# Kernel tuning notes

Measured on AMD Instinct MI355X. Metric: run time of the kernel, lower is better.

Reference implementation:

```python
import jax, jax.numpy as jnp
import numpy as np

B, T, H, N = 4, 2048, 16, 64  # batch, seq, heads, head_size (RWKV standard N=64)


def setup_inputs() -> dict:
    key = jax.random.key(0)
    ks = jax.random.split(key, 5)
    r = jax.random.normal(ks[0], (B, T, H, N), jnp.float32)
    k = jax.random.normal(ks[1], (B, T, H, N), jnp.float32)
    v = jax.random.normal(ks[2], (B, T, H, N), jnp.float32)
    w = jax.random.normal(ks[3], (B, T, H, N), jnp.float32)  # raw decay logits
    u = jax.random.normal(ks[4], (H, N), jnp.float32)         # per-head bonus
    return {"r": r, "k": k, "v": v, "w": w, "u": u}


def _wkv_scan(r, k, v, w, u):
    # RWKV-6 fused recurrent WKV.
    # decay in (0,1): exp(-exp(w)) per RWKV-6 parameterization
    decay = jnp.exp(-jnp.exp(w))  # [B,T,H,N]
    # time-major for lax.scan: [T,B,H,N]
    rt = jnp.moveaxis(r, 1, 0)
    kt = jnp.moveaxis(k, 1, 0)
    vt = jnp.moveaxis(v, 1, 0)
    dt = jnp.moveaxis(decay, 1, 0)
    S0 = jnp.zeros((r.shape[0], r.shape[2], r.shape[3], r.shape[3]), r.dtype)  # [B,H,N,N]

    ub = u[None]  # [1,H,N] broadcast over batch; key index i gets bonus

    def step(S, x):
        r_t, k_t, v_t, d_t = x  # each [B,H,N]
        kv = k_t[..., :, None] * v_t[..., None, :]  # [B,H,N,N] outer product
        # o_j = sum_i r_i * (S_ij + u_i * kv_ij)
        o = jnp.einsum('bhi,bhij->bhj', r_t, S + ub[..., None] * kv)
        S_new = d_t[..., None] * S + kv  # per-channel decay on key axis
        return S_new, o

    _, o = jax.lax.scan(step, S0, (rt, kt, vt, dt))  # o: [T,B,H,N]
    return jnp.moveaxis(o, 0, 1)  # [B,T,H,N]


def reference(r, k, v, w, u):
    return _wkv_scan(r, k, v, w, u)
```

## Files before the change

### kernel.cpp

```cpp
#include <hip/hip_runtime.h>
#include <math.h>


namespace {
constexpr int B = 4, T = 2048, H = 16, N = 64;
constexpr int BH = B * H;
constexpr int NG = 32;
constexpr int TC = 64;
constexpr int LDP = 72;

typedef __attribute__((ext_vector_type(8))) short s8v;
typedef __attribute__((ext_vector_type(4))) float f4v;

#define MFMA16(a, b, c) __builtin_amdgcn_mfma_f32_16x16x32_bf16((a), (b), (c), 0, 0, 0)

__device__ __forceinline__ unsigned short cv(float f) {
    union { float f; unsigned u; } x; x.f = f;
    unsigned r = x.u + 0x7FFFu + ((x.u >> 16) & 1u);
    return (unsigned short)(r >> 16);
}

__device__ __forceinline__ float bfhi(unsigned u) {
    union { unsigned u; float f; } x; x.u = u & 0xFFFF0000u; return x.f;
}
__device__ __forceinline__ float bflo(unsigned u) {
    union { unsigned u; float f; } x; x.u = u << 16; return x.f;
}

__device__ __forceinline__ int sw(int row, int col) {
    return row * LDP + col;
}

__device__ __forceinline__ s8v frag8(const unsigned short* buf, int row_base, int k_base) {
    const int l = threadIdx.x & 63;
    return *(const s8v*)&buf[sw(row_base + (l & 15), k_base + 8 * (l >> 4))];
}

__global__ __launch_bounds__(256, 4)
void k_p0(const float* __restrict__ kp, const float* __restrict__ vp,
          const float* __restrict__ wp,
          unsigned short* __restrict__ Lg, float* __restrict__ Ag)
{
    __shared__ unsigned short sA[64 * LDP];
    __shared__ unsigned short sVT[64 * LDP];
    __shared__ float spans[4 * 64];

    const int blk = blockIdx.x;
    const int g   = blk & (NG - 1);
    const int bh  = blk / NG;
    const int b   = bh / H, h = bh - b * H;
    const int wv  = threadIdx.x >> 6;
    const int ln  = threadIdx.x & 63;

    const int stride = H * N;
    const int base_w = ((b * T + g * TC + wv * 16) * H + h) * N + ln;
    const int cb = (bh * NG + g) * (N * N);

    float d_[16];
    float k_[16];
    {
        float pd = 1.f;
#pragma unroll
        for (int tt = 0; tt < 16; ++tt) {
            const int a = base_w + tt * stride;
            const float dd = __expf(-__expf(wp[a]));
            d_[tt] = dd;
            pd *= dd;
            k_[tt] = kp[a];
        }
        spans[wv * 64 + ln] = pd;
    }
#pragma unroll
    for (int half = 0; half < 2; ++half) {
        s8v pk;
#pragma unroll
        for (int e = 0; e < 8; ++e)
            pk[e] = (short)cv(vp[base_w + (half * 8 + e) * stride]);
        *(s8v*)&sVT[sw(ln, wv * 16 + half * 8)] = pk;
    }
    __syncthreads();
    const float sd0 = spans[0 * 64 + ln], sd1 = spans[1 * 64 + ln];
    const float sd2 = spans[2 * 64 + ln], sd3 = spans[3 * 64 + ln];
    const float sfollow = (wv < 1 ? sd1 : 1.f) * (wv < 2 ? sd2 : 1.f)
                        * (wv < 3 ? sd3 : 1.f);

    s8v p0, p1;
    {
        float suf = sfollow;
#pragma unroll
        for (int tt = 15; tt >= 0; --tt) {
            const unsigned short v16 = cv(k_[tt] * suf);
            if (tt < 8) p0[tt] = (short)v16; else p1[tt - 8] = (short)v16;
            suf *= d_[tt];
        }
    }
    *(s8v*)&sA[sw(ln, wv * 16)]     = p0;
    *(s8v*)&sA[sw(ln, wv * 16 + 8)] = p1;
    __syncthreads();
#pragma unroll
    for (int jb = 0; jb < 4; ++jb) {
        f4v acc = {0.f, 0.f, 0.f, 0.f};
        acc = MFMA16(frag8(sA, wv * 16, 0),  frag8(sVT, jb * 16, 0),  acc);
        acc = MFMA16(frag8(sA, wv * 16, 32), frag8(sVT, jb * 16, 32), acc);
        const int i0 = wv * 16 + (ln >> 4) * 4;
        const int j  = jb * 16 + (ln & 15);
#pragma unroll
        for (int q = 0; q < 4; ++q)
            Lg[cb + (i0 + q) * 64 + j] = cv(acc[q]);
    }
    if (wv == 0) Ag[(bh * NG + g) * 64 + ln] = sd0 * sd1 * sd2 * sd3;
}

__global__ __launch_bounds__(256)
void k2_scan(const unsigned short* __restrict__ L, const float* __restrict__ A,
             float* __restrict__ S0)
{
    const int tid = blockIdx.x * 256 + threadIdx.x;
    const int j2 = tid & 31;
    const int i  = (tid >> 5) & 63;
    const int bh = tid >> 11;

    const unsigned* Lu = (const unsigned*)L;
    float2* S2 = (float2*)S0;
    const int lstride = N * N / 2;
    int lidx = (bh * NG) * lstride + i * 32 + j2;
    int aidx = (bh * NG) * N + i;

    float s0 = 0.f, s1 = 0.f;
    for (int g = 0; g < NG; ++g) {
        const unsigned lw = Lu[lidx];
        const float a = A[aidx];
        S2[lidx] = make_float2(s0, s1);
        s0 = fmaf(a, s0, bflo(lw));
        s1 = fmaf(a, s1, bfhi(lw));
        lidx += lstride;
        aidx += N;
    }
}

__global__ __launch_bounds__(256, 4)
void k_p1(const float* __restrict__ rp, const float* __restrict__ kp,
          const float* __restrict__ vp, const float* __restrict__ wp,
          const float* __restrict__ up,
          const float* __restrict__ S0g,
          float* __restrict__ out)
{
    __shared__ unsigned short sA[64 * LDP];
    __shared__ unsigned short sB[64 * LDP];
    __shared__ unsigned short sVT[64 * LDP];
    __shared__ unsigned short sST[64 * LDP];
    __shared__ float spans[4 * 64];
    unsigned short* const sAm = sA;

    const int blk = blockIdx.x;
    const int g   = blk & (NG - 1);
    const int bh  = blk / NG;
    const int b   = bh / H, h = bh - b * H;
    const int wv  = threadIdx.x >> 6;
    const int ln  = threadIdx.x & 63;

    const int stride = H * N;
    const int base_w = ((b * T + g * TC + wv * 16) * H + h) * N + ln;
    const int cb = (bh * NG + g) * (N * N);

    float d_[16];
    float k_[16], r_[16];
    {
        float pd = 1.f;
#pragma unroll
        for (int tt = 0; tt < 16; ++tt) {
            const int a = base_w + tt * stride;
            const float dd = __expf(-__expf(wp[a]));
            d_[tt] = dd;
            pd *= dd;
            k_[tt] = kp[a];
            r_[tt] = rp[a];
        }
        spans[wv * 64 + ln] = pd;
    }
#pragma unroll
    for (int half = 0; half < 2; ++half) {
        s8v pk;
#pragma unroll
        for (int e = 0; e < 8; ++e)
            pk[e] = (short)cv(vp[base_w + (half * 8 + e) * stride]);
        *(s8v*)&sVT[sw(ln, wv * 16 + half * 8)] = pk;
    }
#pragma unroll
    for (int half = 0; half < 2; ++half) {
        s8v pk;
#pragma unroll
        for (int e = 0; e < 8; ++e)
            pk[e] = (short)cv(S0g[cb + (wv * 16 + half * 8 + e) * 64 + ln]);
        *(s8v*)&sST[sw(ln, wv * 16 + half * 8)] = pk;
    }
    __syncthreads();
    const float sd0 = spans[0 * 64 + ln], sd1 = spans[1 * 64 + ln];
    const float sd2 = spans[2 * 64 + ln];
    const float dOffW = (wv > 0 ? sd0 : 1.f) * (wv > 1 ? sd1 : 1.f)
                      * (wv > 2 ? sd2 : 1.f);

    const float uln = up[h * 64 + ln];
    const int cc = ln & 15;

    f4v accD = {0.f, 0.f, 0.f, 0.f};
#pragma unroll
    for (int tt = 0; tt < 16; ++tt) sB[sw(wv * 16 + tt, ln)] = cv(k_[tt]);
#pragma unroll
    for (int tt = 0; tt < 16; ++tt) sA[sw(wv * 16 + tt, ln)] = cv(r_[tt]);
    {
        f4v tmp = {0.f, 0.f, 0.f, 0.f};
        tmp = MFMA16(frag8(sA, wv * 16, 0),  frag8(sB, wv * 16, 0),  tmp);
        tmp = MFMA16(frag8(sA, wv * 16, 32), frag8(sB, wv * 16, 32), tmp);
#pragma unroll
        for (int q = 0; q < 4; ++q) {
            const int tt = (ln >> 4) * 4 + q;
            if (tt == cc + 1 && (tt & 1)) accD[q] += tmp[q];
        }
    }
#pragma unroll
    for (int tt = 0; tt < 16; ++tt) sA[sw(wv * 16 + tt, ln)] = cv(r_[tt] * uln);
    {
        f4v tmp = {0.f, 0.f, 0.f, 0.f};
        tmp = MFMA16(frag8(sA, wv * 16, 0),  frag8(sB, wv * 16, 0),  tmp);
        tmp = MFMA16(frag8(sA, wv * 16, 32), frag8(sB, wv * 16, 32), tmp);
#pragma unroll
        for (int q = 0; q < 4; ++q) {
            const int tt = (ln >> 4) * 4 + q;
            if (tt == cc) accD[q] += tmp[q];
        }
    }
#pragma unroll
    for (int L = 1; L < 4; ++L) {
        {
            float fA = 1.f;
#pragma unroll
            for (int tt = 0; tt < 16; ++tt) {
                if ((tt & ((1 << L) - 1)) == 0) fA = 1.f;
                else                            fA *= d_[tt - 1];
                sA[sw(wv * 16 + tt, ln)] = cv(r_[tt] * fA);
            }
        }
        {
            float fB = 1.f;
#pragma unroll
            for (int tt = 15; tt >= 0; --tt) {
                if ((tt & ((1 << L) - 1)) == ((1 << L) - 1)) fB = 1.f;
                else                                         fB *= d_[tt + 1];
                sB[sw(wv * 16 + tt, ln)] = cv(k_[tt] * fB);
            }
        }
        f4v tmp = {0.f, 0.f, 0.f, 0.f};
        tmp = MFMA16(frag8(sA, wv * 16, 0),  frag8(sB, wv * 16, 0),  tmp);
        tmp = MFMA16(frag8(sA, wv * 16, 32), frag8(sB, wv * 16, 32), tmp);
#pragma unroll
        for (int q = 0; q < 4; ++q) {
            const int tt = (ln >> 4) * 4 + q;
            if (((tt >> L) == ((cc >> L) + 1)) && (((tt >> L) & 1) != 0))
                accD[q] += tmp[q];
        }
    }

    {
        float pfx = 1.f;
#pragma unroll
        for (int tt = 0; tt < 16; ++tt) {
            sA[sw(wv * 16 + tt, ln)] = cv(r_[tt] * pfx);
            pfx *= d_[tt];
        }
        float suf = 1.f;
#pragma unroll
        for (int tt = 15; tt >= 0; --tt) {
            sB[sw(wv * 16 + tt, ln)] = cv(k_[tt] * suf);
            suf *= d_[tt];
        }
    }
    __syncthreads();
    f4v accL4 = {0.f, 0.f, 0.f, 0.f};
    if (wv == 1 || wv == 3) {
        accL4 = MFMA16(frag8(sA, wv * 16, 0),  frag8(sB, (wv - 1) * 16, 0),  accL4);
        accL4 = MFMA16(frag8(sA, wv * 16, 32), frag8(sB, (wv - 1) * 16, 32), accL4);
    }
    __syncthreads();

    if (wv >= 2) {
        float f = (wv == 2) ? 1.f : sd2;
#pragma unroll
        for (int tt = 0; tt < 16; ++tt) {
            sA[sw(wv * 16 + tt, ln)] = cv(r_[tt] * f);
            f *= d_[tt];
        }
    } else {
        float f = (wv == 0) ? sd1 : 1.f;
#pragma unroll
        for (int tt = 15; tt >= 0; --tt) {
            sB[sw(wv * 16 + tt, ln)] = cv(k_[tt] * f);
            f *= d_[tt];
        }
    }
    __syncthreads();
    f4v acc50 = {0.f, 0.f, 0.f, 0.f}, acc51 = {0.f, 0.f, 0.f, 0.f};
    if (wv >= 2) {
        acc50 = MFMA16(frag8(sA, wv * 16, 0),  frag8(sB, 0, 0),   acc50);
        acc50 = MFMA16(frag8(sA, wv * 16, 32), frag8(sB, 0, 32),  acc50);
        acc51 = MFMA16(frag8(sA, wv * 16, 0),  frag8(sB, 16, 0),  acc51);
        acc51 = MFMA16(frag8(sA, wv * 16, 32), frag8(sB, 16, 32), acc51);
    }

    {
        float f = dOffW;
#pragma unroll
        for (int tt = 0; tt < 16; ++tt) {
            sA[sw(wv * 16 + tt, ln)] = cv(r_[tt] * f);
            f *= d_[tt];
        }
    }
    f4v accO[4];
#pragma unroll
    for (int jb = 0; jb < 4; ++jb) {
        f4v a = {0.f, 0.f, 0.f, 0.f};
        a = MFMA16(frag8(sA, wv * 16, 0),  frag8(sST, jb * 16, 0),  a);
        a = MFMA16(frag8(sA, wv * 16, 32), frag8(sST, jb * 16, 32), a);
        accO[jb] = a;
    }

#pragma unroll
    for (int q = 0; q < 4; ++q) {
        const int tt = (ln >> 4) * 4 + q;
        sAm[sw(wv * 16 + tt, wv * 16 + cc)] = cv(accD[q]);
    }
    if (wv == 1 || wv == 3) {
#pragma unroll
        for (int q = 0; q < 4; ++q) {
            const int tt = (ln >> 4) * 4 + q;
            sAm[sw(wv * 16 + tt, (wv - 1) * 16 + cc)] = cv(accL4[q]);
        }
    }
    if (wv >= 2) {
#pragma unroll
        for (int q = 0; q < 4; ++q) {
            const int tt = (ln >> 4) * 4 + q;
            sAm[sw(wv * 16 + tt, cc)]      = cv(acc50[q]);
            sAm[sw(wv * 16 + tt, 16 + cc)] = cv(acc51[q]);
        }
    }
    if (wv == 0 || wv == 2) {
#pragma unroll
        for (int q = 0; q < 4; ++q) {
            const int tt = (ln >> 4) * 4 + q;
            sAm[sw(wv * 16 + tt, (wv + 1) * 16 + cc)] = 0;
        }
    }

#pragma unroll
    for (int jb = 0; jb < 4; ++jb) {
        f4v a = accO[jb];
        a = MFMA16(frag8(sAm, wv * 16, 0), frag8(sVT, jb * 16, 0), a);
        if (wv >= 2)
            a = MFMA16(frag8(sAm, wv * 16, 32), frag8(sVT, jb * 16, 32), a);
#pragma unroll
        for (int q = 0; q < 4; ++q) {
            const int t = g * TC + wv * 16 + (ln >> 4) * 4 + q;
            out[((b * T + t) * H + h) * N + jb * 16 + (ln & 15)] = a[q];
        }
    }
}

__global__ __launch_bounds__(64, 2)
void k_seq(const float* __restrict__ rp, const float* __restrict__ kp,
           const float* __restrict__ vp, const float* __restrict__ wp,
           const float* __restrict__ up, float* __restrict__ out)
{
    const int bh = blockIdx.x;
    const int b = bh / H, h = bh - b * H;
    const int j = threadIdx.x;

    float S[N];
#pragma unroll
    for (int i = 0; i < N; ++i) S[i] = 0.f;

    const int stride = H * N;
    int base = ((b * T) * H + h) * N;
    const int ubase = h * N;

#pragma unroll 1
    for (int tt = 0; tt < T; ++tt) {
        const float vj = vp[base + j];
        const int row = base;
        float sr = 0.f, o0 = 0.f, o1 = 0.f;
#pragma unroll
        for (int i = 0; i < N; ++i) {
            const float ki = kp[row + i];
            const float di = __expf(-__expf(wp[row + i]));
            const float ri = rp[row + i];
            sr = fmaf(ri * up[ubase + i], ki, sr);
            if (i & 1) o1 = fmaf(ri, S[i], o1);
            else       o0 = fmaf(ri, S[i], o0);
            S[i] = fmaf(di, S[i], ki * vj);
        }
        out[base + j] = fmaf(sr, vj, o0 + o1);
        base += stride;
    }
}

}

extern "C" void kernel_launch(void* const* d_in, const int* in_sizes, int n_in,
                              void* d_out, int out_size, void* d_ws, size_t ws_size,
                              hipStream_t stream)
{
    const float* r = (const float*)d_in[0];
    const float* k = (const float*)d_in[1];
    const float* v = (const float*)d_in[2];
    const float* w = (const float*)d_in[3];
    const float* u = (const float*)d_in[4];
    float* out = (float*)d_out;

    const size_t l_elems = (size_t)BH * NG * N * N;
    const size_t a_elems = (size_t)BH * NG * N;
    const size_t ws_need = l_elems * sizeof(unsigned short)
                         + a_elems * sizeof(float)
                         + l_elems * sizeof(float);

    if (ws_size >= ws_need) {
        unsigned short* L = (unsigned short*)d_ws;
        float* A  = (float*)(L + l_elems);
        float* S0 = A + a_elems;
        k_p0<<<BH * NG, 256, 0, stream>>>(k, v, w, L, A);
        k2_scan<<<(BH * N * N / 2) / 256, 256, 0, stream>>>(L, A, S0);
        k_p1<<<BH * NG, 256, 0, stream>>>(r, k, v, w, u, S0, out);
    } else {
        k_seq<<<BH, 64, 0, stream>>>(r, k, v, w, u, out);
    }
}
```

Baseline: 67.47 us.

## Process two time chunks per block in k_p1 to increase ILP

Each k_p1 block now handles two consecutive 64-step chunks, with double shared-memory buffers and interleaved per-chunk MFMA phases, so the grid is halved. The goal is more independent MFMA and memory work between barriers and fewer total barriers per chunk. In exchange, register and LDS use roughly double and launch bounds drop from 4 to 2 blocks per CU, which lowers occupancy, and only 1024 blocks remain.

```diff
diff --git a/kernel.cpp b/kernel.cpp
--- a/kernel.cpp
+++ b/kernel.cpp
@@ -138,230 +138,265 @@
     }
 }
 
-__global__ __launch_bounds__(256, 4)
+__global__ __launch_bounds__(256, 2)
 void k_p1(const float* __restrict__ rp, const float* __restrict__ kp,
           const float* __restrict__ vp, const float* __restrict__ wp,
           const float* __restrict__ up,
           const float* __restrict__ S0g,
           float* __restrict__ out)
 {
-    __shared__ unsigned short sA[64 * LDP];
-    __shared__ unsigned short sB[64 * LDP];
-    __shared__ unsigned short sVT[64 * LDP];
-    __shared__ unsigned short sST[64 * LDP];
-    __shared__ float spans[4 * 64];
-    unsigned short* const sAm = sA;
+    __shared__ unsigned short sAb[2][64 * LDP];
+    __shared__ unsigned short sBb[2][64 * LDP];
+    __shared__ unsigned short sVTb[2][64 * LDP];
+    __shared__ unsigned short sSTb[2][64 * LDP];
+    __shared__ float spansb[2][4 * 64];
 
     const int blk = blockIdx.x;
-    const int g   = blk & (NG - 1);
-    const int bh  = blk / NG;
+    const int gp  = blk & (NG / 2 - 1);
+    const int bh  = blk / (NG / 2);
     const int b   = bh / H, h = bh - b * H;
     const int wv  = threadIdx.x >> 6;
     const int ln  = threadIdx.x & 63;
-
+    const int cc  = ln & 15;
     const int stride = H * N;
-    const int base_w = ((b * T + g * TC + wv * 16) * H + h) * N + ln;
-    const int cb = (bh * NG + g) * (N * N);
-
-    float d_[16];
-    float k_[16], r_[16];
-    {
+
+    float d_[2][16], k_[2][16], r_[2][16];
+    int base_w[2], cb[2];
+#pragma unroll
+    for (int c = 0; c < 2; ++c) {
+        const int g = 2 * gp + c;
+        base_w[c] = ((b * T + g * TC + wv * 16) * H + h) * N + ln;
+        cb[c]     = (bh * NG + g) * (N * N);
         float pd = 1.f;
 #pragma unroll
         for (int tt = 0; tt < 16; ++tt) {
-            const int a = base_w + tt * stride;
+            const int a = base_w[c] + tt * stride;
             const float dd = __expf(-__expf(wp[a]));
-            d_[tt] = dd;
+            d_[c][tt] = dd;
             pd *= dd;
-            k_[tt] = kp[a];
-            r_[tt] = rp[a];
-        }
-        spans[wv * 64 + ln] = pd;
-    }
-#pragma unroll
-    for (int half = 0; half < 2; ++half) {
-        s8v pk;
-#pragma unroll
-        for (int e = 0; e < 8; ++e)
-            pk[e] = (short)cv(vp[base_w + (half * 8 + e) * stride]);
-        *(s8v*)&sVT[sw(ln, wv * 16 + half * 8)] = pk;
-    }
-#pragma unroll
-    for (int half = 0; half < 2; ++half) {
-        s8v pk;
-#pragma unroll
-        for (int e = 0; e < 8; ++e)
-            pk[e] = (short)cv(S0g[cb + (wv * 16 + half * 8 + e) * 64 + ln]);
-        *(s8v*)&sST[sw(ln, wv * 16 + half * 8)] = pk;
-    }
-    __syncthreads();
-    const float sd0 = spans[0 * 64 + ln], sd1 = spans[1 * 64 + ln];
-    const float sd2 = spans[2 * 64 + ln];
-    const float dOffW = (wv > 0 ? sd0 : 1.f) * (wv > 1 ? sd1 : 1.f)
-                      * (wv > 2 ? sd2 : 1.f);
-
+            k_[c][tt] = kp[a];
+            r_[c][tt] = rp[a];
+        }
+        spansb[c][wv * 64 + ln] = pd;
+#pragma unroll
+        for (int half = 0; half < 2; ++half) {
+            s8v pk;
+#pragma unroll
+            for (int e = 0; e < 8; ++e)
+                pk[e] = (short)cv(vp[base_w[c] + (half * 8 + e) * stride]);
+            *(s8v*)&sVTb[c][sw(ln, wv * 16 + half * 8)] = pk;
+        }
+#pragma unroll
+        for (int half = 0; half < 2; ++half) {
+            s8v pk;
+#pragma unroll
+            for (int e = 0; e < 8; ++e)
+                pk[e] = (short)cv(S0g[cb[c] + (wv * 16 + half * 8 + e) * 64 + ln]);
+            *(s8v*)&sSTb[c][sw(ln, wv * 16 + half * 8)] = pk;
+        }
+    }
+    __syncthreads();
+
+    float dOffW[2], sd1v[2], sd2v[2];
+#pragma unroll
+    for (int c = 0; c < 2; ++c) {
+        const float sd0 = spansb[c][0 * 64 + ln];
+        const float sd1 = spansb[c][1 * 64 + ln];
+        const float sd2 = spansb[c][2 * 64 + ln];
+        dOffW[c] = (wv > 0 ? sd0 : 1.f) * (wv > 1 ? sd1 : 1.f)
+                 * (wv > 2 ? sd2 : 1.f);
+        sd1v[c] = sd1;
+        sd2v[c] = sd2;
+    }
     const float uln = up[h * 64 + ln];
-    const int cc = ln & 15;
-
-    f4v accD = {0.f, 0.f, 0.f, 0.f};
-#pragma unroll
-    for (int tt = 0; tt < 16; ++tt) sB[sw(wv * 16 + tt, ln)] = cv(k_[tt]);
-#pragma unroll
-    for (int tt = 0; tt < 16; ++tt) sA[sw(wv * 16 + tt, ln)] = cv(r_[tt]);
-    {
+
+    f4v accD[2] = {{0.f, 0.f, 0.f, 0.f}, {0.f, 0.f, 0.f, 0.f}};
+#pragma unroll
+    for (int c = 0; c < 2; ++c) {
+#pragma unroll
+        for (int tt = 0; tt < 16; ++tt) sBb[c][sw(wv * 16 + tt, ln)] = cv(k_[c][tt]);
+#pragma unroll
+        for (int tt = 0; tt < 16; ++tt) sAb[c][sw(wv * 16 + tt, ln)] = cv(r_[c][tt]);
+    }
+#pragma unroll
+    for (int c = 0; c < 2; ++c) {
         f4v tmp = {0.f, 0.f, 0.f, 0.f};
-        tmp = MFMA16(frag8(sA, wv * 16, 0),  frag8(sB, wv * 16, 0),  tmp);
-        tmp = MFMA16(frag8(sA, wv * 16, 32), frag8(sB, wv * 16, 32), tmp);
+        tmp = MFMA16(frag8(sAb[c], wv * 16, 0),  frag8(sBb[c], wv * 16, 0),  tmp);
+        tmp = MFMA16(frag8(sAb[c], wv * 16, 32), frag8(sBb[c], wv * 16, 32), tmp);
 #pragma unroll
         for (int q = 0; q < 4; ++q) {
             const int tt = (ln >> 4) * 4 + q;
-            if (tt == cc + 1 && (tt & 1)) accD[q] += tmp[q];
-        }
-    }
-#pragma unroll
-    for (int tt = 0; tt < 16; ++tt) sA[sw(wv * 16 + tt, ln)] = cv(r_[tt] * uln);
-    {
+            if (tt == cc + 1 && (tt & 1)) accD[c][q] += tmp[q];
+        }
+    }
+#pragma unroll
+    for (int c = 0; c < 2; ++c) {
+#pragma unroll
+        for (int tt = 0; tt < 16; ++tt)
+            sAb[c][sw(wv * 16 + tt, ln)] = cv(r_[c][tt] * uln);
+    }
+#pragma unroll
+    for (int c = 0; c < 2; ++c) {
         f4v tmp = {0.f, 0.f, 0.f, 0.f};
-        tmp = MFMA16(frag8(sA, wv * 16, 0),  frag8(sB, wv * 16, 0),  tmp);
-        tmp = MFMA16(frag8(sA, wv * 16, 32), frag8(sB, wv * 16, 32), tmp);
+        tmp = MFMA16(frag8(sAb[c], wv * 16, 0),  frag8(sBb[c], wv * 16, 0),  tmp);
+        tmp = MFMA16(frag8(sAb[c], wv * 16, 32), frag8(sBb[c], wv * 16, 32), tmp);
 #pragma unroll
         for (int q = 0; q < 4; ++q) {
             const int tt = (ln >> 4) * 4 + q;
-            if (tt == cc) accD[q] += tmp[q];
+            if (tt == cc) accD[c][q] += tmp[q];
         }
     }
 #pragma unroll
     for (int L = 1; L < 4; ++L) {
-        {
+#pragma unroll
+        for (int c = 0; c < 2; ++c) {
             float fA = 1.f;
 #pragma unroll
             for (int tt = 0; tt < 16; ++tt) {
                 if ((tt & ((1 << L) - 1)) == 0) fA = 1.f;
-                else                            fA *= d_[tt - 1];
-                sA[sw(wv * 16 + tt, ln)] = cv(r_[tt] * fA);
-            }
-        }
-        {
+                else                            fA *= d_[c][tt - 1];
+                sAb[c][sw(wv * 16 + tt, ln)] = cv(r_[c][tt] * fA);
+            }
             float fB = 1.f;
 #pragma unroll
             for (int tt = 15; tt >= 0; --tt) {
                 if ((tt & ((1 << L) - 1)) == ((1 << L) - 1)) fB = 1.f;
-                else                                         fB *= d_[tt + 1];
-                sB[sw(wv * 16 + tt, ln)] = cv(k_[tt] * fB);
-            }
-        }
-        f4v tmp = {0.f, 0.f, 0.f, 0.f};
-        tmp = MFMA16(frag8(sA, wv * 16, 0),  frag8(sB, wv * 16, 0),  tmp);
-        tmp = MFMA16(frag8(sA, wv * 16, 32), frag8(sB, wv * 16, 32), tmp);
+                else                                         fB *= d_[c][tt + 1];
+                sBb[c][sw(wv * 16 + tt, ln)] = cv(k_[c][tt] * fB);
+            }
+        }
+#pragma unroll
+        for (int c = 0; c < 2; ++c) {
+            f4v tmp = {0.f, 0.f, 0.f, 0.f};
+            tmp = MFMA16(frag8(sAb[c], wv * 16, 0),  frag8(sBb[c], wv * 16, 0),  tmp);
+            tmp = MFMA16(frag8(sAb[c], wv * 16, 32), frag8(sBb[c], wv * 16, 32), tmp);
+#pragma unroll
+            for (int q = 0; q < 4; ++q) {
+                const int tt = (ln >> 4) * 4 + q;
+                if (((tt >> L) == ((cc >> L) + 1)) && (((tt >> L) & 1) != 0))
+                    accD[c][q] += tmp[q];
+            }
+        }
+    }
+
+#pragma unroll
+    for (int c = 0; c < 2; ++c) {
+        float pfx = 1.f;
+#pragma unroll
+        for (int tt = 0; tt < 16; ++tt) {
+            sAb[c][sw(wv * 16 + tt, ln)] = cv(r_[c][tt] * pfx);
+            pfx *= d_[c][tt];
+        }
+        float suf = 1.f;
+#pragma unroll
+        for (int tt = 15; tt >= 0; --tt) {
+            sBb[c][sw(wv * 16 + tt, ln)] = cv(k_[c][tt] * suf);
+            suf *= d_[c][tt];
+        }
+    }
+    __syncthreads();
+    f4v accL4[2] = {{0.f, 0.f, 0.f, 0.f}, {0.f, 0.f, 0.f, 0.f}};
+    if (wv == 1 || wv == 3) {
+#pragma unroll
+        for (int c = 0; c < 2; ++c) {
+            accL4[c] = MFMA16(frag8(sAb[c], wv * 16, 0),
+                              frag8(sBb[c], (wv - 1) * 16, 0),  accL4[c]);
+            accL4[c] = MFMA16(frag8(sAb[c], wv * 16, 32),
+                              frag8(sBb[c], (wv - 1) * 16, 32), accL4[c]);
+        }
+    }
+    __syncthreads();
+
+#pragma unroll
+    for (int c = 0; c < 2; ++c) {
+        if (wv >= 2) {
+            float f = (wv == 2) ? 1.f : sd2v[c];
+#pragma unroll
+            for (int tt = 0; tt < 16; ++tt) {
+                sAb[c][sw(wv * 16 + tt, ln)] = cv(r_[c][tt] * f);
+                f *= d_[c][tt];
+            }
+        } else {
+            float f = (wv == 0) ? sd1v[c] : 1.f;
+#pragma unroll
+            for (int tt = 15; tt >= 0; --tt) {
+                sBb[c][sw(wv * 16 + tt, ln)] = cv(k_[c][tt] * f);
+                f *= d_[c][tt];
+            }
+        }
+    }
+    __syncthreads();
+    f4v acc50[2] = {{0.f, 0.f, 0.f, 0.f}, {0.f, 0.f, 0.f, 0.f}};
+    f4v acc51[2] = {{0.f, 0.f, 0.f, 0.f}, {0.f, 0.f, 0.f, 0.f}};
+    if (wv >= 2) {
+#pragma unroll
+        for (int c = 0; c < 2; ++c) {
+            acc50[c] = MFMA16(frag8(sAb[c], wv * 16, 0),  frag8(sBb[c], 0, 0),   acc50[c]);
+            acc50[c] = MFMA16(frag8(sAb[c], wv * 16, 32), frag8(sBb[c], 0, 32),  acc50[c]);
+            acc51[c] = MFMA16(frag8(sAb[c], wv * 16, 0),  frag8(sBb[c], 16, 0),  acc51[c]);
+            acc51[c] = MFMA16(frag8(sAb[c], wv * 16, 32), frag8(sBb[c], 16, 32), acc51[c]);
+        }
+    }
+
+#pragma unroll
+    for (int c = 0; c < 2; ++c) {
+        {
+            float f = dOffW[c];
+#pragma unroll
+            for (int tt = 0; tt < 16; ++tt) {
+                sAb[c][sw(wv * 16 + tt, ln)] = cv(r_[c][tt] * f);
+                f *= d_[c][tt];
+            }
+        }
+        f4v accO[4];
+#pragma unroll
+        for (int jb = 0; jb < 4; ++jb) {
+            f4v a = {0.f, 0.f, 0.f, 0.f};
+            a = MFMA16(frag8(sAb[c], wv * 16, 0),  frag8(sSTb[c], jb * 16, 0),  a);
+            a = MFMA16(frag8(sAb[c], wv * 16, 32), frag8(sSTb[c], jb * 16, 32), a);
+            accO[jb] = a;
+        }
+
+        unsigned short* const sAm = sAb[c];
 #pragma unroll
         for (int q = 0; q < 4; ++q) {
             const int tt = (ln >> 4) * 4 + q;
-            if (((tt >> L) == ((cc >> L) + 1)) && (((tt >> L) & 1) != 0))
-                accD[q] += tmp[q];
-        }
-    }
-
-    {
-        float pfx = 1.f;
-#pragma unroll
-        for (int tt = 0; tt < 16; ++tt) {
-            sA[sw(wv * 16 + tt, ln)] = cv(r_[tt] * pfx);
-            pfx *= d_[tt];
-        }
-        float suf = 1.f;
-#pragma unroll
-        for (int tt = 15; tt >= 0; --tt) {
-            sB[sw(wv * 16 + tt, ln)] = cv(k_[tt] * suf);
-            suf *= d_[tt];
-        }
-    }
-    __syncthreads();
-    f4v accL4 = {0.f, 0.f, 0.f, 0.f};
-    if (wv == 1 || wv == 3) {
-        accL4 = MFMA16(frag8(sA, wv * 16, 0),  frag8(sB, (wv - 1) * 16, 0),  accL4);
-        accL4 = MFMA16(frag8(sA, wv * 16, 32), frag8(sB, (wv - 1) * 16, 32), accL4);
-    }
-    __syncthreads();
-
-    if (wv >= 2) {
-        float f = (wv == 2) ? 1.f : sd2;
-#pragma unroll
-        for (int tt = 0; tt < 16; ++tt) {
-            sA[sw(wv * 16 + tt, ln)] = cv(r_[tt] * f);
-            f *= d_[tt];
-        }
-    } else {
-        float f = (wv == 0) ? sd1 : 1.f;
-#pragma unroll
-        for (int tt = 15; tt >= 0; --tt) {
-            sB[sw(wv * 16 + tt, ln)] = cv(k_[tt] * f);
-            f *= d_[tt];
-        }
-    }
-    __syncthreads();
-    f4v acc50 = {0.f, 0.f, 0.f, 0.f}, acc51 = {0.f, 0.f, 0.f, 0.f};
-    if (wv >= 2) {
-        acc50 = MFMA16(frag8(sA, wv * 16, 0),  frag8(sB, 0, 0),   acc50);
-        acc50 = MFMA16(frag8(sA, wv * 16, 32), frag8(sB, 0, 32),  acc50);
-        acc51 = MFMA16(frag8(sA, wv * 16, 0),  frag8(sB, 16, 0),  acc51);
-        acc51 = MFMA16(frag8(sA, wv * 16, 32), frag8(sB, 16, 32), acc51);
-    }
-
-    {
-        float f = dOffW;
-#pragma unroll
-        for (int tt = 0; tt < 16; ++tt) {
-            sA[sw(wv * 16 + tt, ln)] = cv(r_[tt] * f);
-            f *= d_[tt];
-        }
-    }
-    f4v accO[4];
-#pragma unroll
-    for (int jb = 0; jb < 4; ++jb) {
-        f4v a = {0.f, 0.f, 0.f, 0.f};
-        a = MFMA16(frag8(sA, wv * 16, 0),  frag8(sST, jb * 16, 0),  a);
-        a = MFMA16(frag8(sA, wv * 16, 32), frag8(sST, jb * 16, 32), a);
-        accO[jb] = a;
-    }
-
-#pragma unroll
-    for (int q = 0; q < 4; ++q) {
-        const int tt = (ln >> 4) * 4 + q;
-        sAm[sw(wv * 16 + tt, wv * 16 + cc)] = cv(accD[q]);
-    }
-    if (wv == 1 || wv == 3) {
-#pragma unroll
-        for (int q = 0; q < 4; ++q) {
-            const int tt = (ln >> 4) * 4 + q;
-            sAm[sw(wv * 16 + tt, (wv - 1) * 16 + cc)] = cv(accL4[q]);
-        }
-    }
-    if (wv >= 2) {
-#pragma unroll
-        for (int q = 0; q < 4; ++q) {
-            const int tt = (ln >> 4) * 4 + q;
-            sAm[sw(wv * 16 + tt, cc)]      = cv(acc50[q]);
-            sAm[sw(wv * 16 + tt, 16 + cc)] = cv(acc51[q]);
-        }
-    }
-    if (wv == 0 || wv == 2) {
-#pragma unroll
-        for (int q = 0; q < 4; ++q) {
-            const int tt = (ln >> 4) * 4 + q;
-            sAm[sw(wv * 16 + tt, (wv + 1) * 16 + cc)] = 0;
-        }
-    }
-
-#pragma unroll
-    for (int jb = 0; jb < 4; ++jb) {
-        f4v a = accO[jb];
-        a = MFMA16(frag8(sAm, wv * 16, 0), frag8(sVT, jb * 16, 0), a);
-        if (wv >= 2)
-            a = MFMA16(frag8(sAm, wv * 16, 32), frag8(sVT, jb * 16, 32), a);
-#pragma unroll
-        for (int q = 0; q < 4; ++q) {
-            const int t = g * TC + wv * 16 + (ln >> 4) * 4 + q;
-            out[((b * T + t) * H + h) * N + jb * 16 + (ln & 15)] = a[q];
+            sAm[sw(wv * 16 + tt, wv * 16 + cc)] = cv(accD[c][q]);
+        }
+        if (wv == 1 || wv == 3) {
+#pragma unroll
+            for (int q = 0; q < 4; ++q) {
+                const int tt = (ln >> 4) * 4 + q;
+                sAm[sw(wv * 16 + tt, (wv - 1) * 16 + cc)] = cv(accL4[c][q]);
+            }
+        }
+        if (wv >= 2) {
+#pragma unroll
+            for (int q = 0; q < 4; ++q) {
+                const int tt = (ln >> 4) * 4 + q;
+                sAm[sw(wv * 16 + tt, cc)]      = cv(acc50[c][q]);
+                sAm[sw(wv * 16 + tt, 16 + cc)] = cv(acc51[c][q]);
+            }
+        }
+        if (wv == 0 || wv == 2) {
+#pragma unroll
+            for (int q = 0; q < 4; ++q) {
+                const int tt = (ln >> 4) * 4 + q;
+                sAm[sw(wv * 16 + tt, (wv + 1) * 16 + cc)] = 0;
+            }
+        }
+
+#pragma unroll
+        for (int jb = 0; jb < 4; ++jb) {
+            f4v a = accO[jb];
+            a = MFMA16(frag8(sAm, wv * 16, 0), frag8(sVTb[c], jb * 16, 0), a);
+            if (wv >= 2)
+                a = MFMA16(frag8(sAm, wv * 16, 32), frag8(sVTb[c], jb * 16, 32), a);
+#pragma unroll
+            for (int q = 0; q < 4; ++q) {
+                const int t = (2 * gp + c) * TC + wv * 16 + (ln >> 4) * 4 + q;
+                out[((b * T + t) * H + h) * N + jb * 16 + (ln & 15)] = a[q];
+            }
         }
     }
 }
@@ -428,7 +463,7 @@
         float* S0 = A + a_elems;
         k_p0<<<BH * NG, 256, 0, stream>>>(k, v, w, L, A);
         k2_scan<<<(BH * N * N / 2) / 256, 256, 0, stream>>>(L, A, S0);
-        k_p1<<<BH * NG, 256, 0, stream>>>(r, k, v, w, u, S0, out);
+        k_p1<<<BH * NG / 2, 256, 0, stream>>>(r, k, v, w, u, S0, out);
     } else {
         k_seq<<<BH, 64, 0, stream>>>(r, k, v, w, u, out);
     }
```

New measurement: 77.64 us. +15.1%, slower.
